# Optimization experiments

Measured on AMD Instinct MI355X. Metric: run time of the kernel, lower is better.

Reference implementation:

```python
import jax, jax.numpy as jnp
import numpy as np

# Haar (db1) analysis filters, matching the torch buffers exactly.
_SQRT2_INV = 0.7071067811865476
_H0 = jnp.array([_SQRT2_INV, _SQRT2_INV], dtype=jnp.float32)
_H1 = jnp.array([-_SQRT2_INV, _SQRT2_INV], dtype=jnp.float32)


def setup_inputs() -> dict:
    key = jax.random.key(0)
    x = jax.random.normal(key, (16, 3, 1024, 1024), dtype=jnp.float32)
    return {
        "x": x,
        "h0_h": _H0.reshape(1, 1, 1, 2),  # horizontal lowpass  (OIHW)
        "h1_h": _H1.reshape(1, 1, 1, 2),  # horizontal highpass
        "h0_v": _H0.reshape(1, 1, 2, 1),  # vertical lowpass
        "h1_v": _H1.reshape(1, 1, 2, 1),  # vertical highpass
    }


def _conv(x, k, stride):
    # torch F.conv2d == cross-correlation; lax conv is also cross-correlation (no flip).
    return jax.lax.conv_general_dilated(
        x, k, window_strides=stride, padding="VALID",
        dimension_numbers=("NCHW", "OIHW", "NCHW"))


def _dwt(x, h0_h, h1_h, h0_v, h1_v):
    B, C, H, W = x.shape
    taps = h0_h.shape[-1]
    pad = taps - 1
    # zero-pad on the left (width), then horizontal filtering with stride 2 in W
    xp = jnp.pad(x, ((0, 0), (0, 0), (0, 0), (pad, 0))).reshape(B * C, 1, H, W + pad)
    x_h0 = _conv(xp, h0_h, (1, 2))  # (B*C,1,H,W_out)
    x_h1 = _conv(xp, h1_h, (1, 2))
    # zero-pad on the top (height), then vertical filtering with stride 2 in H
    x_h0 = jnp.pad(x_h0, ((0, 0), (0, 0), (pad, 0), (0, 0)))
    x_h1 = jnp.pad(x_h1, ((0, 0), (0, 0), (pad, 0), (0, 0)))
    LL = _conv(x_h0, h0_v, (2, 1))
    LH = _conv(x_h0, h1_v, (2, 1))
    HL = _conv(x_h1, h0_v, (2, 1))
    HH = _conv(x_h1, h1_v, (2, 1))
    Hf, Wf = LL.shape[-2], LL.shape[-1]
    rs = lambda t: t.reshape(B, C, Hf, Wf)
    return rs(LL), (rs(LH), rs(HL), rs(HH))


def reference(x, h0_h, h1_h, h0_v, h1_v):
    return _dwt(x, h0_h, h1_h, h0_v, h1_v)
```

## Files before the change

kernel.cpp:

```cpp
#include <hip/hip_runtime.h>


__global__ __launch_bounds__(256) void dwt_haar_kernel(
    const float* __restrict__ x, float* __restrict__ out, int n_bc)
{
    constexpr int W  = 1024;
    constexpr int Ho = 512;
    constexpr int Wo = 512;
    constexpr int J4 = Wo / 4;

    const long long S = (long long)n_bc * Ho * Wo;

    int g   = blockIdx.x * 256 + threadIdx.x;
    int j4  = g & (J4 - 1);
    int rem = g >> 7;
    int i   = rem & (Ho - 1);
    int bc  = rem >> 9;

    const float* rbot = x + ((long long)bc * 1024 + 2 * i) * W;
    const int c0 = j4 << 3;

    float bot[9], top[9];
    {
        float4 v0 = *(const float4*)(rbot + c0);
        float4 v1 = *(const float4*)(rbot + c0 + 4);
        bot[1] = v0.x; bot[2] = v0.y; bot[3] = v0.z; bot[4] = v0.w;
        bot[5] = v1.x; bot[6] = v1.y; bot[7] = v1.z; bot[8] = v1.w;
        bot[0] = (j4 > 0) ? rbot[c0 - 1] : 0.0f;
    }
    if (i > 0) {
        const float* rtop = rbot - W;
        float4 v0 = *(const float4*)(rtop + c0);
        float4 v1 = *(const float4*)(rtop + c0 + 4);
        top[1] = v0.x; top[2] = v0.y; top[3] = v0.z; top[4] = v0.w;
        top[5] = v1.x; top[6] = v1.y; top[7] = v1.z; top[8] = v1.w;
        top[0] = (j4 > 0) ? rtop[c0 - 1] : 0.0f;
    } else {
#pragma unroll
        for (int k = 0; k < 9; ++k) top[k] = 0.0f;
    }

    float llv[4], lhv[4], hlv[4], hhv[4];
#pragma unroll
    for (int k = 0; k < 4; ++k) {
        float a = top[2 * k], b = top[2 * k + 1];
        float c = bot[2 * k], d = bot[2 * k + 1];
        float sum_t = a + b, dif_t = b - a;
        float sum_b = c + d, dif_b = d - c;
        llv[k] = 0.5f * (sum_t + sum_b);
        lhv[k] = 0.5f * (sum_b - sum_t);
        hlv[k] = 0.5f * (dif_t + dif_b);
        hhv[k] = 0.5f * (dif_b - dif_t);
    }

    const long long obase = ((long long)bc * Ho + i) * Wo + (j4 << 2);
    *(float4*)(out +         obase) = make_float4(llv[0], llv[1], llv[2], llv[3]);
    *(float4*)(out +     S + obase) = make_float4(lhv[0], lhv[1], lhv[2], lhv[3]);
    *(float4*)(out + 2 * S + obase) = make_float4(hlv[0], hlv[1], hlv[2], hlv[3]);
    *(float4*)(out + 3 * S + obase) = make_float4(hhv[0], hhv[1], hhv[2], hhv[3]);
}

extern "C" void kernel_launch(void* const* d_in, const int* in_sizes, int n_in,
                              void* d_out, int out_size, void* d_ws, size_t ws_size,
                              hipStream_t stream) {
    const float* x = (const float*)d_in[0];
    float* out = (float*)d_out;

    const int n_bc = in_sizes[0] / (1024 * 1024);
    const long long total_threads = (long long)n_bc * 512 * 128;
    const int blocks = (int)(total_threads / 256);

    dwt_haar_kernel<<<blocks, 256, 0, stream>>>(x, out, n_bc);
}
```

Baseline: 336.4 us.

## Remap threads to one output row per block with shuffled halo and nontemporal stores

Each block now handles a single output row, and each thread loads one float4 per input row instead of two. The left-neighbor halo value comes from a warp shuffle rather than an extra scalar global load; only lane 0 still reads it from memory. Outputs are written as float2 nontemporal stores so the write-once results bypass cache. The aim is fewer redundant loads and less cache pollution, at the cost of narrower stores and twice as many threads doing less work each.

Result: no change. 341.2 us (+1.4%).

```diff
diff --git a/kernel.cpp b/kernel.cpp
--- a/kernel.cpp
+++ b/kernel.cpp
@@ -1,63 +1,60 @@
 #include <hip/hip_runtime.h>
 
+
+typedef float v2f __attribute__((ext_vector_type(2)));
 
 __global__ __launch_bounds__(256) void dwt_haar_kernel(
     const float* __restrict__ x, float* __restrict__ out, int n_bc)
 {
-    constexpr int W  = 1024;
-    constexpr int Ho = 512;
-    constexpr int Wo = 512;
-    constexpr int J4 = Wo / 4;
+    const int i    = blockIdx.x & 511;
+    const int bc   = blockIdx.x >> 9;
+    const int t    = threadIdx.x;
+    const int lane = t & 63;
+    const int c0   = t << 2;
 
-    const long long S = (long long)n_bc * Ho * Wo;
+    const long long S = (long long)n_bc * 512 * 512;
 
-    int g   = blockIdx.x * 256 + threadIdx.x;
-    int j4  = g & (J4 - 1);
-    int rem = g >> 7;
-    int i   = rem & (Ho - 1);
-    int bc  = rem >> 9;
+    const float* rbot = x + (((long long)bc << 10) + 2 * i) * 1024;
 
-    const float* rbot = x + ((long long)bc * 1024 + 2 * i) * W;
-    const int c0 = j4 << 3;
+    float4 vb = *(const float4*)(rbot + c0);
+    float  pb = __shfl_up(vb.w, 1);
+    if (lane == 0) pb = (t > 0) ? rbot[c0 - 1] : 0.0f;
 
-    float bot[9], top[9];
-    {
-        float4 v0 = *(const float4*)(rbot + c0);
-        float4 v1 = *(const float4*)(rbot + c0 + 4);
-        bot[1] = v0.x; bot[2] = v0.y; bot[3] = v0.z; bot[4] = v0.w;
-        bot[5] = v1.x; bot[6] = v1.y; bot[7] = v1.z; bot[8] = v1.w;
-        bot[0] = (j4 > 0) ? rbot[c0 - 1] : 0.0f;
-    }
+    float4 vt;
+    float  pt;
     if (i > 0) {
-        const float* rtop = rbot - W;
-        float4 v0 = *(const float4*)(rtop + c0);
-        float4 v1 = *(const float4*)(rtop + c0 + 4);
-        top[1] = v0.x; top[2] = v0.y; top[3] = v0.z; top[4] = v0.w;
-        top[5] = v1.x; top[6] = v1.y; top[7] = v1.z; top[8] = v1.w;
-        top[0] = (j4 > 0) ? rtop[c0 - 1] : 0.0f;
+        const float* rtop = rbot - 1024;
+        vt = *(const float4*)(rtop + c0);
+        pt = __shfl_up(vt.w, 1);
+        if (lane == 0) pt = (t > 0) ? rtop[c0 - 1] : 0.0f;
     } else {
-#pragma unroll
-        for (int k = 0; k < 9; ++k) top[k] = 0.0f;
+        vt = make_float4(0.0f, 0.0f, 0.0f, 0.0f);
+        pt = 0.0f;
     }
 
-    float llv[4], lhv[4], hlv[4], hhv[4];
-#pragma unroll
-    for (int k = 0; k < 4; ++k) {
-        float a = top[2 * k], b = top[2 * k + 1];
-        float c = bot[2 * k], d = bot[2 * k + 1];
-        float sum_t = a + b, dif_t = b - a;
-        float sum_b = c + d, dif_b = d - c;
-        llv[k] = 0.5f * (sum_t + sum_b);
-        lhv[k] = 0.5f * (sum_b - sum_t);
-        hlv[k] = 0.5f * (dif_t + dif_b);
-        hhv[k] = 0.5f * (dif_b - dif_t);
+    v2f llv, lhv, hlv, hhv;
+    {
+        float st = pt + vt.x, dt = vt.x - pt;
+        float sb = pb + vb.x, db = vb.x - pb;
+        llv.x = 0.5f * (st + sb);
+        lhv.x = 0.5f * (sb - st);
+        hlv.x = 0.5f * (dt + db);
+        hhv.x = 0.5f * (db - dt);
+    }
+    {
+        float st = vt.y + vt.z, dt = vt.z - vt.y;
+        float sb = vb.y + vb.z, db = vb.z - vb.y;
+        llv.y = 0.5f * (st + sb);
+        lhv.y = 0.5f * (sb - st);
+        hlv.y = 0.5f * (dt + db);
+        hhv.y = 0.5f * (db - dt);
     }
 
-    const long long obase = ((long long)bc * Ho + i) * Wo + (j4 << 2);
-    *(float4*)(out +         obase) = make_float4(llv[0], llv[1], llv[2], llv[3]);
-    *(float4*)(out +     S + obase) = make_float4(lhv[0], lhv[1], lhv[2], lhv[3]);
-    *(float4*)(out + 2 * S + obase) = make_float4(hlv[0], hlv[1], hlv[2], hlv[3]);
-    *(float4*)(out + 3 * S + obase) = make_float4(hhv[0], hhv[1], hhv[2], hhv[3]);
+    const long long obase = (((long long)bc << 9) + i) * 512 + (t << 1);
+    __builtin_nontemporal_store(llv, (v2f*)(out +         obase));
+    __builtin_nontemporal_store(lhv, (v2f*)(out +     S + obase));
+    __builtin_nontemporal_store(hlv, (v2f*)(out + 2 * S + obase));
+    __builtin_nontemporal_store(hhv, (v2f*)(out + 3 * S + obase));
 }
 
 extern "C" void kernel_launch(void* const* d_in, const int* in_sizes, int n_in,
@@ -66,9 +63,8 @@
     const float* x = (const float*)d_in[0];
     float* out = (float*)d_out;
 
-    const int n_bc = in_sizes[0] / (1024 * 1024);
-    const long long total_threads = (long long)n_bc * 512 * 128;
-    const int blocks = (int)(total_threads / 256);
+    const int n_bc   = in_sizes[0] / (1024 * 1024);
+    const int blocks = n_bc * 512;
 
     dwt_haar_kernel<<<blocks, 256, 0, stream>>>(x, out, n_bc);
 }
```
